# Kernel optimization log

Measured on AMD Instinct MI355X. Metric: run time of the kernel, lower is better.

The kernel has to match this reference:

```python
import jax, jax.numpy as jnp
import numpy as np

N_VERTS = 40962  # icosphere level-6 vertex count
K_RING = 19      # 2-ring filter size


def setup_inputs() -> dict:
    key = jax.random.key(0)
    k1, k2, k3, k4 = jax.random.split(key, 4)
    B, C_in, C_out = 4, 64, 64
    x = jax.random.normal(k1, (B, C_in, N_VERTS), dtype=jnp.float32)
    neigh_orders = jax.random.randint(k2, (N_VERTS, K_RING), 0, N_VERTS, dtype=jnp.int32)
    # nn.Linear(19*in_feats, out_feats): weight [C_out, 19*C_in], bias [C_out]
    fan_in = K_RING * C_in
    bound = 1.0 / np.sqrt(fan_in)
    W = jax.random.uniform(k3, (C_out, fan_in), dtype=jnp.float32, minval=-bound, maxval=bound)
    b = jax.random.uniform(k4, (C_out,), dtype=jnp.float32, minval=-bound, maxval=bound)
    return {"x": x, "neigh_orders": neigh_orders, "W": W, "b": b}


def reference(x, neigh_orders, W, b):
    # x: [B, C_in, N] -> [B, N, C_in]
    xt = jnp.transpose(x, (0, 2, 1))
    B, N, C = xt.shape
    # gather 19-ring neighbors: [B, N, 19, C_in]
    gathered = xt[:, neigh_orders, :]
    # im2col-style flatten: [B, N, 19*C_in]
    mat = gathered.reshape(B, N, K_RING * C)
    # Linear: mat @ W.T + b -> [B, N, C_out]
    out = jnp.einsum('bnk,ok->bno', mat, W) + b
    # back to [B, C_out, N]
    return jnp.transpose(out, (0, 2, 1))
```

## Files before the change

kernel.cpp:

```cpp
#include <hip/hip_runtime.h>
#include <hip/hip_bf16.h>


#define NV   40962
#define KR   19
#define CIN  64
#define COUT 64
#define NB   4

typedef __bf16 bf16;
typedef __bf16 bf16x8 __attribute__((ext_vector_type(8)));
typedef float  floatx4 __attribute__((ext_vector_type(4)));

#define XT_ELEMS ((size_t)NB * NV * CIN)
#define WB_OFF   ((XT_ELEMS * 2 + 255) & ~(size_t)255)
#define WS_NEED  (WB_OFF + (size_t)COUT * KR * CIN * 2)

__global__ __launch_bounds__(256) void transpose_kernel(
    const float* __restrict__ x, bf16* __restrict__ xt)
{
    __shared__ alignas(16) bf16 tile[64 * 72];
    const int b  = blockIdx.y;
    const int v0 = blockIdx.x * 64;
    const int t  = threadIdx.x;
    const int vl = t & 63;
    const int c0 = t >> 6;

    const int vg = min(v0 + vl, NV - 1);
    #pragma unroll
    for (int p = 0; p < 16; ++p) {
        int c = c0 + p * 4;
        tile[vl * 72 + c] = (bf16)x[((size_t)(b * CIN + c)) * NV + vg];
    }
    __syncthreads();

    const int v = t >> 2;
    #pragma unroll
    for (int p = 0; p < 2; ++p) {
        int chunk = (t & 3) + p * 4;
        if (v0 + v < NV) {
            *(bf16x8*)&xt[((size_t)(b * NV + v0 + v)) * 64 + chunk * 8] =
                *(bf16x8*)&tile[v * 72 + chunk * 8];
        }
    }
}

__global__ __launch_bounds__(256) void convw_kernel(
    const float* __restrict__ W, bf16* __restrict__ Wb)
{
    int i = blockIdx.x * 256 + threadIdx.x;
    const int total4 = COUT * KR * CIN / 4;
    if (i < total4) {
        float4 v = ((const float4*)W)[i];
        bf16* p = Wb + (size_t)i * 4;
        p[0] = (bf16)v.x; p[1] = (bf16)v.y; p[2] = (bf16)v.z; p[3] = (bf16)v.w;
    }
}

__global__ __launch_bounds__(256, 3) void conv_kernel(
    const int*   __restrict__ neigh,
    const bf16*  __restrict__ xt,
    const bf16*  __restrict__ Wb,
    const float* __restrict__ bias,
    float*       __restrict__ out)
{
    __shared__ alignas(16) bf16 Wlds[64 * 72];

    const int b    = blockIdx.y;
    const int n0   = blockIdx.x * 256;
    const int t    = threadIdx.x;
    const int wv   = t >> 6;
    const int lane = t & 63;
    const int l15  = lane & 15;
    const int g    = lane >> 4;

    int nn[4], ib[4];
    #pragma unroll
    for (int s = 0; s < 4; ++s) {
        nn[s] = n0 + wv * 64 + s * 16 + l15;
        ib[s] = min(nn[s], NV - 1) * KR;
    }

    floatx4 acc[4][4];
    #pragma unroll
    for (int s = 0; s < 4; ++s)
        #pragma unroll
        for (int o = 0; o < 4; ++o)
            acc[s][o] = (floatx4){0.f, 0.f, 0.f, 0.f};

    const int wo = t >> 2;
    const int wc = t & 3;

    for (int r = 0; r < KR; ++r) {
        bf16x8 xf[4][2];
        #pragma unroll
        for (int s = 0; s < 4; ++s) {
            int v = neigh[ib[s] + r];
            v = ((unsigned)v < (unsigned)NV) ? v : 0;
            const bf16* p = xt + (((size_t)(b * NV + v)) << 6) + g * 8;
            xf[s][0] = *(const bf16x8*)(p);
            xf[s][1] = *(const bf16x8*)(p + 32);
        }

        __syncthreads();
        #pragma unroll
        for (int p2 = 0; p2 < 2; ++p2) {
            int chunk = wc + p2 * 4;
            *(bf16x8*)&Wlds[wo * 72 + chunk * 8] =
                *(const bf16x8*)&Wb[(size_t)wo * (KR * 64) + r * 64 + chunk * 8];
        }
        __syncthreads();

        #pragma unroll
        for (int ot = 0; ot < 4; ++ot) {
            #pragma unroll
            for (int kc = 0; kc < 2; ++kc) {
                bf16x8 wf = *(const bf16x8*)
                    &Wlds[(ot * 16 + l15) * 72 + kc * 32 + g * 8];
                #pragma unroll
                for (int s = 0; s < 4; ++s) {
                    acc[s][ot] = __builtin_amdgcn_mfma_f32_16x16x32_bf16(
                        wf, xf[s][kc], acc[s][ot], 0, 0, 0);
                }
            }
        }
    }

    #pragma unroll
    for (int ot = 0; ot < 4; ++ot) {
        #pragma unroll
        for (int i = 0; i < 4; ++i) {
            int o = ot * 16 + g * 4 + i;
            float bv = bias[o];
            #pragma unroll
            for (int s = 0; s < 4; ++s) {
                if (nn[s] < NV) {
                    out[((size_t)(b * COUT + o)) * NV + nn[s]] =
                        acc[s][ot][i] + bv;
                }
            }
        }
    }
}

__global__ __launch_bounds__(64) void fallback_kernel(
    const int*   __restrict__ neigh,
    const float* __restrict__ x,
    const float* __restrict__ W,
    const float* __restrict__ bias,
    float*       __restrict__ out)
{
    __shared__ float xg[KR * CIN];
    const int bn = blockIdx.x;
    const int b  = bn / NV;
    const int n  = bn % NV;
    const int t  = threadIdx.x;

    for (int k = t; k < KR * CIN; k += 64) {
        int r = k / CIN, c = k - r * CIN;
        int v = neigh[n * KR + r];
        v = ((unsigned)v < (unsigned)NV) ? v : 0;
        xg[k] = x[((size_t)(b * CIN + c)) * NV + v];
    }
    __syncthreads();

    float s = bias[t];
    const float* wrow = W + (size_t)t * (KR * CIN);
    for (int k = 0; k < KR * CIN; ++k) s += xg[k] * wrow[k];
    out[((size_t)(b * COUT + t)) * NV + n] = s;
}

extern "C" void kernel_launch(void* const* d_in, const int* in_sizes, int n_in,
                              void* d_out, int out_size, void* d_ws, size_t ws_size,
                              hipStream_t stream)
{
    const float* x     = (const float*)d_in[0];
    const int*   neigh = (const int*)d_in[1];
    const float* W     = (const float*)d_in[2];
    const float* bias  = (const float*)d_in[3];
    float* out = (float*)d_out;

    if (d_ws != nullptr && ws_size >= WS_NEED) {
        bf16* xt = (bf16*)d_ws;
        bf16* Wb = (bf16*)((char*)d_ws + WB_OFF);

        dim3 tgrid((NV + 63) / 64, NB);
        transpose_kernel<<<tgrid, 256, 0, stream>>>(x, xt);
        convw_kernel<<<(COUT * KR * CIN / 4 + 255) / 256, 256, 0, stream>>>(W, Wb);

        dim3 cgrid((NV + 255) / 256, NB);
        conv_kernel<<<cgrid, 256, 0, stream>>>(neigh, xt, Wb, bias, out);
    } else {
        fallback_kernel<<<NB * NV, 64, 0, stream>>>(neigh, x, W, bias, out);
    }
}
```

Baseline: 187.9 us.

## Software-pipeline ring gathers with double-buffered weights and smaller conv tiles

The conv kernel now prefetches the next ring's gathered features into registers and the next weight slice into a second LDS buffer while running MFMAs on the current one, which cuts the barriers per ring from two to one. Tiles shrink from 256 to 128 vertices per block, with a remapped 1D grid that interleaves batches and tiles and raises the occupancy hint to 4. The transpose kernel now stages fp32 in a padded LDS tile and converts to bf16 on the way out. The cost is more blocks, each doing less MFMA work per weight slice loaded, plus extra registers for the prefetch buffers.

```diff
diff --git a/kernel.cpp b/kernel.cpp
--- a/kernel.cpp
+++ b/kernel.cpp
@@ -7,6 +7,7 @@
 #define CIN  64
 #define COUT 64
 #define NB   4
+#define NTILES 321
 
 typedef __bf16 bf16;
 typedef __bf16 bf16x8 __attribute__((ext_vector_type(8)));
@@ -19,28 +20,32 @@
 __global__ __launch_bounds__(256) void transpose_kernel(
     const float* __restrict__ x, bf16* __restrict__ xt)
 {
-    __shared__ alignas(16) bf16 tile[64 * 72];
+    __shared__ float tile[64 * 65];
     const int b  = blockIdx.y;
     const int v0 = blockIdx.x * 64;
     const int t  = threadIdx.x;
+
     const int vl = t & 63;
     const int c0 = t >> 6;
-
     const int vg = min(v0 + vl, NV - 1);
     #pragma unroll
     for (int p = 0; p < 16; ++p) {
-        int c = c0 + p * 4;
-        tile[vl * 72 + c] = (bf16)x[((size_t)(b * CIN + c)) * NV + vg];
+        int c = c0 * 16 + p;
+        tile[vl * 65 + c] = x[((size_t)(b * CIN + c)) * NV + vg];
     }
     __syncthreads();
 
     const int v = t >> 2;
-    #pragma unroll
-    for (int p = 0; p < 2; ++p) {
-        int chunk = (t & 3) + p * 4;
-        if (v0 + v < NV) {
-            *(bf16x8*)&xt[((size_t)(b * NV + v0 + v)) * 64 + chunk * 8] =
-                *(bf16x8*)&tile[v * 72 + chunk * 8];
+    const int q = t & 3;
+    if (v0 + v < NV) {
+        #pragma unroll
+        for (int p = 0; p < 2; ++p) {
+            int chunk = q + p * 4;
+            bf16x8 o;
+            #pragma unroll
+            for (int j = 0; j < 8; ++j)
+                o[j] = (bf16)tile[v * 65 + chunk * 8 + j];
+            *(bf16x8*)&xt[((size_t)(b * NV + v0 + v)) * 64 + chunk * 8] = o;
         }
     }
 }
@@ -57,33 +62,37 @@
     }
 }
 
-__global__ __launch_bounds__(256, 3) void conv_kernel(
+__global__ __launch_bounds__(256, 4) void conv_kernel(
     const int*   __restrict__ neigh,
     const bf16*  __restrict__ xt,
     const bf16*  __restrict__ Wb,
     const float* __restrict__ bias,
     float*       __restrict__ out)
 {
-    __shared__ alignas(16) bf16 Wlds[64 * 72];
-
-    const int b    = blockIdx.y;
-    const int n0   = blockIdx.x * 256;
+    __shared__ alignas(16) bf16 Wlds[2][64 * 72];
+
+    const int i    = blockIdx.x;
+    const int b    = (i & 7) >> 1;
+    const int tile = (i >> 3) * 2 + (i & 1);
+    if (tile >= NTILES) return;
+    const int n0   = tile * 128;
+
     const int t    = threadIdx.x;
     const int wv   = t >> 6;
     const int lane = t & 63;
     const int l15  = lane & 15;
     const int g    = lane >> 4;
 
-    int nn[4], ib[4];
-    #pragma unroll
-    for (int s = 0; s < 4; ++s) {
-        nn[s] = n0 + wv * 64 + s * 16 + l15;
+    int nn[2], ib[2];
+    #pragma unroll
+    for (int s = 0; s < 2; ++s) {
+        nn[s] = n0 + wv * 32 + s * 16 + l15;
         ib[s] = min(nn[s], NV - 1) * KR;
     }
 
-    floatx4 acc[4][4];
-    #pragma unroll
-    for (int s = 0; s < 4; ++s)
+    floatx4 acc[2][4];
+    #pragma unroll
+    for (int s = 0; s < 2; ++s)
         #pragma unroll
         for (int o = 0; o < 4; ++o)
             acc[s][o] = (floatx4){0.f, 0.f, 0.f, 0.f};
@@ -91,52 +100,73 @@
     const int wo = t >> 2;
     const int wc = t & 3;
 
+    #pragma unroll
+    for (int p2 = 0; p2 < 2; ++p2) {
+        int chunk = wc + p2 * 4;
+        *(bf16x8*)&Wlds[0][wo * 72 + chunk * 8] =
+            *(const bf16x8*)&Wb[(size_t)wo * (KR * 64) + chunk * 8];
+    }
+    bf16x8 xfc[2][2], xfn[2][2];
+    #pragma unroll
+    for (int s = 0; s < 2; ++s) {
+        int v = neigh[ib[s]];
+        v = ((unsigned)v < (unsigned)NV) ? v : 0;
+        const bf16* p = xt + (((size_t)(b * NV + v)) << 6) + g * 8;
+        xfc[s][0] = *(const bf16x8*)(p);
+        xfc[s][1] = *(const bf16x8*)(p + 32);
+    }
+    __syncthreads();
+
     for (int r = 0; r < KR; ++r) {
-        bf16x8 xf[4][2];
-        #pragma unroll
-        for (int s = 0; s < 4; ++s) {
-            int v = neigh[ib[s] + r];
-            v = ((unsigned)v < (unsigned)NV) ? v : 0;
-            const bf16* p = xt + (((size_t)(b * NV + v)) << 6) + g * 8;
-            xf[s][0] = *(const bf16x8*)(p);
-            xf[s][1] = *(const bf16x8*)(p + 32);
-        }
-
-        __syncthreads();
-        #pragma unroll
-        for (int p2 = 0; p2 < 2; ++p2) {
-            int chunk = wc + p2 * 4;
-            *(bf16x8*)&Wlds[wo * 72 + chunk * 8] =
-                *(const bf16x8*)&Wb[(size_t)wo * (KR * 64) + r * 64 + chunk * 8];
-        }
-        __syncthreads();
+        if (r + 1 < KR) {
+            #pragma unroll
+            for (int s = 0; s < 2; ++s) {
+                int v = neigh[ib[s] + r + 1];
+                v = ((unsigned)v < (unsigned)NV) ? v : 0;
+                const bf16* p = xt + (((size_t)(b * NV + v)) << 6) + g * 8;
+                xfn[s][0] = *(const bf16x8*)(p);
+                xfn[s][1] = *(const bf16x8*)(p + 32);
+            }
+            #pragma unroll
+            for (int p2 = 0; p2 < 2; ++p2) {
+                int chunk = wc + p2 * 4;
+                *(bf16x8*)&Wlds[(r + 1) & 1][wo * 72 + chunk * 8] =
+                    *(const bf16x8*)&Wb[(size_t)wo * (KR * 64) + (r + 1) * 64 + chunk * 8];
+            }
+        }
 
         #pragma unroll
         for (int ot = 0; ot < 4; ++ot) {
             #pragma unroll
             for (int kc = 0; kc < 2; ++kc) {
                 bf16x8 wf = *(const bf16x8*)
-                    &Wlds[(ot * 16 + l15) * 72 + kc * 32 + g * 8];
+                    &Wlds[r & 1][(ot * 16 + l15) * 72 + kc * 32 + g * 8];
                 #pragma unroll
-                for (int s = 0; s < 4; ++s) {
+                for (int s = 0; s < 2; ++s) {
                     acc[s][ot] = __builtin_amdgcn_mfma_f32_16x16x32_bf16(
-                        wf, xf[s][kc], acc[s][ot], 0, 0, 0);
+                        wf, xfc[s][kc], acc[s][ot], 0, 0, 0);
                 }
             }
         }
+        __syncthreads();
+        #pragma unroll
+        for (int s = 0; s < 2; ++s) {
+            xfc[s][0] = xfn[s][0];
+            xfc[s][1] = xfn[s][1];
+        }
     }
 
     #pragma unroll
     for (int ot = 0; ot < 4; ++ot) {
         #pragma unroll
-        for (int i = 0; i < 4; ++i) {
-            int o = ot * 16 + g * 4 + i;
+        for (int ii = 0; ii < 4; ++ii) {
+            int o = ot * 16 + g * 4 + ii;
             float bv = bias[o];
             #pragma unroll
-            for (int s = 0; s < 4; ++s) {
+            for (int s = 0; s < 2; ++s) {
                 if (nn[s] < NV) {
                     out[((size_t)(b * COUT + o)) * NV + nn[s]] =
-                        acc[s][ot][i] + bv;
+                        acc[s][ot][ii] + bv;
                 }
             }
         }
@@ -188,8 +218,8 @@
         transpose_kernel<<<tgrid, 256, 0, stream>>>(x, xt);
         convw_kernel<<<(COUT * KR * CIN / 4 + 255) / 256, 256, 0, stream>>>(W, Wb);
 
-        dim3 cgrid((NV + 255) / 256, NB);
-        conv_kernel<<<cgrid, 256, 0, stream>>>(neigh, xt, Wb, bias, out);
+        int nblk = 8 * ((NTILES + 1) / 2);
+        conv_kernel<<<nblk, 256, 0, stream>>>(neigh, xt, Wb, bias, out);
     } else {
         fallback_kernel<<<NB * NV, 64, 0, stream>>>(neigh, x, W, bias, out);
     }
```

Result: faster. 170.2 us (-9.4%).
